# Performance work log

Hardware: AMD Instinct MI355X
Metric: run time of the kernel (lower is better)

## Reference

```python
import jax, jax.numpy as jnp
import numpy as np

B, S, D, F, E, SH, K = 2, 2048, 2048, 1024, 16, 2, 2


def setup_inputs() -> dict:
    key = jax.random.key(0)
    ks = jax.random.split(key, 8)
    std = 0.02
    mk = lambda k, sh: (jax.random.normal(k, sh, jnp.float32) * std)
    return {
        "x": jax.random.normal(ks[0], (B, S, D), jnp.float32),
        "wa": mk(ks[1], (D, E)),                      # router, no bias
        "rg": mk(ks[2], (E, D, F)), "rgb": jnp.zeros((E, F), jnp.float32),
        "rw1": mk(ks[3], (E, D, F)), "rb1": jnp.zeros((E, F), jnp.float32),
        "rw2": mk(ks[4], (E, F, D)), "rb2": jnp.zeros((E, D), jnp.float32),
        "sg": mk(ks[5], (SH, D, F)), "sgb": jnp.zeros((SH, F), jnp.float32),
        "sw1": mk(ks[6], (SH, D, F)), "sb1": jnp.zeros((SH, F), jnp.float32),
        "sw2": mk(ks[7], (SH, F, D)), "sb2": jnp.zeros((SH, D), jnp.float32),
    }


def _experts_all(x, g, gb, w1, b1, w2, b2):
    """Run every expert in the stack on every token.
    x: [b,s,d]; g,w1: [e,d,f]; w2: [e,f,d] -> out [b,s,e,d].
    Expert: w2( gelu(gated(x)) * w1(x) ). torch GELU default = exact erf.
    """
    y = jax.nn.gelu(jnp.einsum('bsd,edf->bsef', x, g) + gb, approximate=False)
    y = y * (jnp.einsum('bsd,edf->bsef', x, w1) + b1)
    return jnp.einsum('bsef,efd->bsed', y, w2) + b2


def reference(x, wa, rg, rgb, rw1, rb1, rw2, rb2, sg, sgb, sw1, sb1, sw2, sb2):
    # sigmoid affinity router + top-k, renormalized over the k selected
    aff = jax.nn.sigmoid(jnp.einsum('bsd,de->bse', x, wa))
    topk_p, topk_i = jax.lax.top_k(aff, K)                   # [b,s,k]
    topk_p = topk_p / jnp.sum(topk_p, axis=-1, keepdims=True)
    # dense combine weights [b,s,E]; zero for unselected experts, so the
    # masked-scatter of the original is reproduced exactly by a weighted sum
    combine = jnp.sum(jax.nn.one_hot(topk_i, E, dtype=x.dtype) * topk_p[..., None], axis=2)
    routed = jnp.einsum('bsed,bse->bsd',
                        _experts_all(x, rg, rgb, rw1, rb1, rw2, rb2), combine)
    shared = jnp.sum(_experts_all(x, sg, sgb, sw1, sb1, sw2, sb2), axis=2)
    return x + shared + routed
```

## Files before the change

### kernel.cpp

```cpp
#include <hip/hip_runtime.h>
#include <hip/hip_bf16.h>
#include <math.h>

typedef __bf16 bf16;
typedef bf16  bf16x8 __attribute__((ext_vector_type(8)));
typedef bf16  bf16x4 __attribute__((ext_vector_type(4)));
typedef float f32x4  __attribute__((ext_vector_type(4)));

#define TOKENS 4096
#define DM 2048
#define FF 1024
#define NE 16
#define SH_BASE 12288
#define BK 64

#define WS_CNT    0
#define WS_POS    64
#define WS_BASE   128
#define WS_TOPKW  256
#define WS_TOPKI  33024
#define WS_TSLOT  65792
#define WS_LIST   98560
#define WS_XB     180480
#define WS_H      16957696
#define WS_Y      58900736
#define WS_B1R    142786816
#define WS_B1S    277004544
#define WS_W2TR   293781760
#define WS_W2TS   360890624

__device__ __forceinline__ bf16 f2bf(float f) {
  unsigned u = __builtin_bit_cast(unsigned, f);
  u += 0x7fffu + ((u >> 16) & 1u);
  unsigned short h = (unsigned short)(u >> 16);
  return __builtin_bit_cast(bf16, h);
}

typedef const __attribute__((address_space(1))) void* gas_t;
typedef __attribute__((address_space(3))) void* las_t;
__device__ __forceinline__ void load_lds16(const bf16* g, bf16* l) {
  __builtin_amdgcn_global_load_lds((gas_t)g, (las_t)l, 16, 0, 0);
}

__global__ void transpose_cvt_all_kernel(const float* __restrict__ rw2, const float* __restrict__ sw2,
                                         bf16* __restrict__ W2TR, bf16* __restrict__ W2TS) {
  __shared__ float tile[64][65];
  const int z = blockIdx.z;
  const float* src_base;
  bf16* dst_base;
  if (z < NE) { src_base = rw2 + (size_t)z * FF * DM; dst_base = W2TR + (size_t)z * DM * FF; }
  else { const int s = z - NE; src_base = sw2 + (size_t)s * FF * DM; dst_base = W2TS + (size_t)s * DM * FF; }
  const int R = FF, C = DM;
  const int c0 = blockIdx.x * 64, r0 = blockIdx.y * 64;
  const int t = threadIdx.x;
  const int lr = t >> 2;
  const int lc = (t & 3) * 4;
  const float* src = src_base + (size_t)(r0 + lr) * C + c0;
#pragma unroll
  for (int j = 0; j < 4; j++) {
    const f32x4 v = *(const f32x4*)(src + lc + j * 16);
    tile[lr][lc + j * 16 + 0] = v[0];
    tile[lr][lc + j * 16 + 1] = v[1];
    tile[lr][lc + j * 16 + 2] = v[2];
    tile[lr][lc + j * 16 + 3] = v[3];
  }
  __syncthreads();
  const int co = t >> 4;
  const int ro = (t & 15) * 4;
#pragma unroll
  for (int j = 0; j < 4; j++) {
    const int c = co + j * 16;
    bf16x4 v;
    v[0] = f2bf(tile[ro + 0][c]);
    v[1] = f2bf(tile[ro + 1][c]);
    v[2] = f2bf(tile[ro + 2][c]);
    v[3] = f2bf(tile[ro + 3][c]);
    *(bf16x4*)(dst_base + (size_t)(c0 + c) * R + r0 + ro) = v;
  }
}

__global__ void transpose_cvt_fused_all_kernel(
    const float* __restrict__ rg, const float* __restrict__ rw1,
    const float* __restrict__ sg, const float* __restrict__ sw1,
    bf16* __restrict__ B1R, bf16* __restrict__ B1S) {
  __shared__ float tile[64][65];
  const int z = blockIdx.z;
  const int half = (z >= 18) ? 1 : 0;
  const int ze = z - 18 * half;
  const float* src_base;
  bf16* dst_base;
  if (ze < NE) {
    src_base = (half ? rw1 : rg) + (size_t)ze * DM * FF;
    dst_base = B1R + (size_t)ze * (2 * FF) * DM;
  } else {
    const int s = ze - NE;
    src_base = (half ? sw1 : sg) + (size_t)s * DM * FF;
    dst_base = B1S + (size_t)s * (2 * FF) * DM;
  }
  const int c0 = blockIdx.x * 64, r0 = blockIdx.y * 64;
  const int t = threadIdx.x;
  const int lr = t >> 2;
  const int lc = (t & 3) * 4;
  const float* src = src_base + (size_t)(r0 + lr) * FF + c0;
#pragma unroll
  for (int j = 0; j < 4; j++) {
    const f32x4 v = *(const f32x4*)(src + lc + j * 16);
    tile[lr][lc + j * 16 + 0] = v[0];
    tile[lr][lc + j * 16 + 1] = v[1];
    tile[lr][lc + j * 16 + 2] = v[2];
    tile[lr][lc + j * 16 + 3] = v[3];
  }
  __syncthreads();
  const int co = t >> 4;
  const int ro = (t & 15) * 4;
#pragma unroll
  for (int j = 0; j < 4; j++) {
    const int c = co + j * 16;
    const int f = c0 + c;
    const int fr = ((f >> 4) << 5) + half * 16 + (f & 15);
    bf16x4 v;
    v[0] = f2bf(tile[ro + 0][c]);
    v[1] = f2bf(tile[ro + 1][c]);
    v[2] = f2bf(tile[ro + 2][c]);
    v[3] = f2bf(tile[ro + 3][c]);
    *(bf16x4*)(dst_base + (size_t)fr * DM + r0 + ro) = v;
  }
}

#define RT_TOK 16
#define RT_DK  256
#define RT_PITCH (RT_DK + 4)

__global__ __launch_bounds__(256) void router_kernel(
    const float* __restrict__ x, const float* __restrict__ wa,
    float* __restrict__ topk_w, int* __restrict__ topk_i,
    int* __restrict__ cnt, bf16* __restrict__ xb) {
  __shared__ float xs[RT_TOK][RT_PITCH];
  __shared__ float was[NE][RT_PITCH];
  __shared__ float aff[RT_TOK][17];

  const int tid = threadIdx.x;
  const int t = tid >> 4;
  const int e = tid & 15;
  const int t0 = blockIdx.x * RT_TOK;

  f32x4 acc4 = {0.f, 0.f, 0.f, 0.f};

  for (int d0 = 0; d0 < DM; d0 += RT_DK) {
    __syncthreads();
    {
      const int r = tid >> 4;
      const int c4 = (tid & 15) * 4;
      const float* src = x + (size_t)(t0 + r) * DM + d0;
      bf16* dstx = xb + (size_t)(t0 + r) * DM + d0;
#pragma unroll
      for (int j = 0; j < 4; j++) {
        const f32x4 v = *(const f32x4*)(src + c4 + j * 64);
        *(f32x4*)(&xs[r][c4 + j * 64]) = v;
        bf16x4 o;
        o[0] = f2bf(v[0]); o[1] = f2bf(v[1]); o[2] = f2bf(v[2]); o[3] = f2bf(v[3]);
        *(bf16x4*)(dstx + c4 + j * 64) = o;
      }
    }
    {
      const int e2 = tid & 15;
      const int dd = (tid >> 4) * 16;
#pragma unroll
      for (int j = 0; j < 16; j++)
        was[e2][dd + j] = wa[(size_t)(d0 + dd + j) * NE + e2];
    }
    __syncthreads();
#pragma unroll 16
    for (int d = 0; d < RT_DK; d += 4) {
      const f32x4 xv = *(const f32x4*)(&xs[t][d]);
      const f32x4 wv = *(const f32x4*)(&was[e][d]);
      acc4 += xv * wv;
    }
  }

  const float a = acc4[0] + acc4[1] + acc4[2] + acc4[3];
  aff[t][e] = 1.f / (1.f + expf(-a));
  __syncthreads();

  if (e == 0) {
    float b0 = -1e30f, b1 = -1e30f; int i0 = 0, i1 = 0;
    for (int i = 0; i < NE; i++) {
      const float v = aff[t][i];
      if (v > b0) { b1 = b0; i1 = i0; b0 = v; i0 = i; }
      else if (v > b1) { b1 = v; i1 = i; }
    }
    const int tok = t0 + t;
    const float inv = 1.f / (b0 + b1);
    topk_w[tok * 2] = b0 * inv;  topk_w[tok * 2 + 1] = b1 * inv;
    topk_i[tok * 2] = i0;        topk_i[tok * 2 + 1] = i1;
    atomicAdd(&cnt[i0], 1);      atomicAdd(&cnt[i1], 1);
  }
}

__global__ void prefix_kernel(const int* __restrict__ cnt, int* __restrict__ base) {
  if (threadIdx.x == 0) {
    int acc = 0;
    for (int e = 0; e < NE; e++) { base[e] = acc; acc += (cnt[e] + 127) & ~127; }
    base[NE] = SH_BASE;
    base[NE + 1] = SH_BASE + TOKENS;
  }
}

__global__ void build_lists_kernel(const int* __restrict__ topk_i, const int* __restrict__ base,
                                   int* __restrict__ pos, int* __restrict__ list,
                                   int* __restrict__ token_slot) {
  const int t = blockIdx.x * 256 + threadIdx.x;
  if (t >= TOKENS) return;
#pragma unroll
  for (int k = 0; k < 2; k++) {
    const int e = topk_i[t * 2 + k];
    const int p = atomicAdd(&pos[e], 1);
    const int slot = base[e] + p;
    list[slot] = t;
    token_slot[t * 2 + k] = slot;
  }
  list[SH_BASE + t] = t;
  list[SH_BASE + TOKENS + t] = t;
}

#define GEMM_GRID_MAX 2304

__device__ __forceinline__ bool map_tile(int flat, const int* __restrict__ cnt,
                                         int& e, int& my, int& nx) {
  int o = 0;
  for (int ee = 0; ee < NE + 2; ++ee) {
    const int ce = (ee < NE) ? cnt[ee] : TOKENS;
    const int me = (ce + 127) >> 7;
    const int Te = me << 4;
    if (flat < o + Te) {
      const int l = flat - o;
      const int s = (l & 7) * (me << 1) + (l >> 3);
      nx = s / me;
      my = s - nx * me;
      e = ee;
      return true;
    }
    o += Te;
  }
  return false;
}

__global__ __launch_bounds__(256, 2) void gemm1_kernel(
    const bf16* __restrict__ xb, const int* __restrict__ list,
    const int* __restrict__ base, const int* __restrict__ cnt,
    const bf16* __restrict__ B1R, const bf16* __restrict__ B1S,
    const float* __restrict__ rgb, const float* __restrict__ rb1,
    const float* __restrict__ sgb, const float* __restrict__ sb1,
    bf16* __restrict__ H) {
  int e, bmy, bnx;
  if (!map_tile(blockIdx.x, cnt, e, bmy, bnx)) return;
  const int ce = (e < NE) ? cnt[e] : TOKENS;
  const int m0 = bmy * 128;
  const int n0 = bnx * 128;
  const int bse = base[e];

  const bf16* B1; const float *gb, *ub;
  if (e < NE) { B1 = B1R + (size_t)e * (2 * FF) * DM; gb = rgb + e * FF; ub = rb1 + e * FF; }
  else { const int s = e - NE; B1 = B1S + (size_t)s * (2 * FF) * DM; gb = sgb + s * FF; ub = sb1 + s * FF; }

  __shared__ bf16 As[2][128 * BK];
  __shared__ bf16 Bs[2][128 * BK];

  const int tid = threadIdx.x, lane = tid & 63, wid = tid >> 6;
  const int lrow = lane >> 3;
  const int laneK = (((lane & 7) ^ lrow) << 3);
  const int q0 = wid << 5;

  const bf16* aP[4];
#pragma unroll
  for (int i = 0; i < 4; i++) {
    int rA = m0 + q0 + (i << 3) + lrow;
    if (rA >= ce) rA = ce - 1;
    aP[i] = xb + (size_t)list[bse + rA] * DM + laneK;
  }
  const bf16* bP = B1 + (size_t)(n0 + q0 + lrow) * DM + laneK;

  const int wm = (wid & 1) * 64, wn = (wid >> 1) * 64;
  const int m16 = lane & 15, quad = lane >> 4, xor7 = m16 & 7;

  f32x4 acc[4][4] = {};

#pragma unroll
  for (int i = 0; i < 4; i++) {
    load_lds16(aP[i], &As[0][(q0 + (i << 3)) * BK + (lane << 3)]);
    load_lds16(bP + (size_t)(i * 8) * DM, &Bs[0][(q0 + (i << 3)) * BK + (lane << 3)]);
  }

  int cur = 0;
  for (int k0 = 0; k0 < DM; k0 += BK) {
    __syncthreads();
    if (k0 + BK < DM) {
      const int nxt = cur ^ 1;
      const int kn = k0 + BK;
#pragma unroll
      for (int i = 0; i < 4; i++) {
        load_lds16(aP[i] + kn, &As[nxt][(q0 + (i << 3)) * BK + (lane << 3)]);
        load_lds16(bP + (size_t)(i * 8) * DM + kn, &Bs[nxt][(q0 + (i << 3)) * BK + (lane << 3)]);
      }
    }
#pragma unroll
    for (int kk = 0; kk < 2; kk++) {
      const int slot = (((kk << 2) + quad) ^ xor7) << 3;
      bf16x8 af[4], bfr[4];
#pragma unroll
      for (int i = 0; i < 4; i++) {
        af[i]  = *(const bf16x8*)(&As[cur][(wm + m16 + 16 * i) * BK + slot]);
        bfr[i] = *(const bf16x8*)(&Bs[cur][(wn + m16 + 16 * i) * BK + slot]);
      }
#pragma unroll
      for (int mi = 0; mi < 4; mi++)
#pragma unroll
        for (int ni = 0; ni < 4; ni++)
          acc[mi][ni] = __builtin_amdgcn_mfma_f32_16x16x32_bf16(af[mi], bfr[ni], acc[mi][ni], 0, 0, 0);
    }
    cur ^= 1;
  }

  const int q4 = quad * 4;
  const int fbase = ((n0 + wn) >> 1) + m16;
#pragma unroll
  for (int mi = 0; mi < 4; mi++) {
#pragma unroll
    for (int nj = 0; nj < 2; nj++) {
      const int f = fbase + nj * 16;
      const float gbv = gb[f], ubv = ub[f];
#pragma unroll
      for (int r = 0; r < 4; r++) {
        const int row = m0 + wm + mi * 16 + q4 + r;
        const float g = acc[mi][2 * nj][r] + gbv;
        const float u = acc[mi][2 * nj + 1][r] + ubv;
        const float h = 0.5f * g * (1.f + erff(g * 0.70710678118f)) * u;
        H[(size_t)(bse + row) * FF + f] = f2bf(h);
      }
    }
  }
}

__global__ __launch_bounds__(256, 2) void gemm2_kernel(
    const bf16* __restrict__ Hb, const int* __restrict__ base, const int* __restrict__ cnt,
    const bf16* __restrict__ rw2T, const bf16* __restrict__ sw2T,
    const float* __restrict__ rb2, const float* __restrict__ sb2,
    bf16* __restrict__ Y) {
  int e, bmy, bnx;
  if (!map_tile(blockIdx.x, cnt, e, bmy, bnx)) return;
  const int m0 = bmy * 128;
  const int n0 = bnx * 128;
  const int bse = base[e];

  const bf16* B; const float* bb;
  if (e < NE) { B = rw2T + (size_t)e * DM * FF; bb = rb2 + e * DM; }
  else { const int s = e - NE; B = sw2T + (size_t)s * DM * FF; bb = sb2 + s * DM; }

  __shared__ bf16 As[2][128 * BK];
  __shared__ bf16 Bs[2][128 * BK];

  const int tid = threadIdx.x, lane = tid & 63, wid = tid >> 6;
  const int lrow = lane >> 3;
  const int laneK = (((lane & 7) ^ lrow) << 3);
  const int q0 = wid << 5;

  const bf16* aP = Hb + (size_t)(bse + m0 + q0 + lrow) * FF + laneK;
  const bf16* bP = B  + (size_t)(n0 + q0 + lrow) * FF + laneK;

  const int wm = (wid & 1) * 64, wn = (wid >> 1) * 64;
  const int m16 = lane & 15, quad = lane >> 4, xor7 = m16 & 7;

  f32x4 acc[4][4] = {};

#pragma unroll
  for (int i = 0; i < 4; i++) {
    load_lds16(aP + (size_t)(i * 8) * FF, &As[0][(q0 + (i << 3)) * BK + (lane << 3)]);
    load_lds16(bP + (size_t)(i * 8) * FF, &Bs[0][(q0 + (i << 3)) * BK + (lane << 3)]);
  }

  int cur = 0;
  for (int k0 = 0; k0 < FF; k0 += BK) {
    __syncthreads();
    if (k0 + BK < FF) {
      const int nxt = cur ^ 1;
      const int kn = k0 + BK;
#pragma unroll
      for (int i = 0; i < 4; i++) {
        load_lds16(aP + (size_t)(i * 8) * FF + kn, &As[nxt][(q0 + (i << 3)) * BK + (lane << 3)]);
        load_lds16(bP + (size_t)(i * 8) * FF + kn, &Bs[nxt][(q0 + (i << 3)) * BK + (lane << 3)]);
      }
    }
#pragma unroll
    for (int kk = 0; kk < 2; kk++) {
      const int slot = (((kk << 2) + quad) ^ xor7) << 3;
      bf16x8 af[4], bfr[4];
#pragma unroll
      for (int i = 0; i < 4; i++) {
        af[i]  = *(const bf16x8*)(&As[cur][(wm + m16 + 16 * i) * BK + slot]);
        bfr[i] = *(const bf16x8*)(&Bs[cur][(wn + m16 + 16 * i) * BK + slot]);
      }
#pragma unroll
      for (int mi = 0; mi < 4; mi++)
#pragma unroll
        for (int ni = 0; ni < 4; ni++)
          acc[mi][ni] = __builtin_amdgcn_mfma_f32_16x16x32_bf16(af[mi], bfr[ni], acc[mi][ni], 0, 0, 0);
    }
    cur ^= 1;
  }

  const int q4 = quad * 4;
#pragma unroll
  for (int mi = 0; mi < 4; mi++) {
#pragma unroll
    for (int ni = 0; ni < 4; ni++) {
      const int n = n0 + wn + ni * 16 + m16;
      const float bv = bb[n];
#pragma unroll
      for (int r = 0; r < 4; r++) {
        const int row = m0 + wm + mi * 16 + q4 + r;
        Y[(size_t)(bse + row) * DM + n] = f2bf(acc[mi][ni][r] + bv);
      }
    }
  }
}

__global__ void combine_kernel(const float* __restrict__ x, const bf16* __restrict__ Y,
                               const int* __restrict__ token_slot, const float* __restrict__ topk_w,
                               float* __restrict__ out) {
  const int t = blockIdx.x;
  const int d = threadIdx.x * 8;
  const int s0 = token_slot[t * 2], s1 = token_slot[t * 2 + 1];
  const float w0 = topk_w[t * 2], w1 = topk_w[t * 2 + 1];
  const bf16x8 ya = *(const bf16x8*)(Y + (size_t)(SH_BASE + t) * DM + d);
  const bf16x8 yb = *(const bf16x8*)(Y + (size_t)(SH_BASE + TOKENS + t) * DM + d);
  const bf16x8 y0 = *(const bf16x8*)(Y + (size_t)s0 * DM + d);
  const bf16x8 y1 = *(const bf16x8*)(Y + (size_t)s1 * DM + d);
  const float* xp = x + (size_t)t * DM + d;
  float* op = out + (size_t)t * DM + d;
#pragma unroll
  for (int j = 0; j < 8; j++)
    op[j] = xp[j] + (float)ya[j] + (float)yb[j] + w0 * (float)y0[j] + w1 * (float)y1[j];
}

extern "C" void kernel_launch(void* const* d_in, const int* in_sizes, int n_in,
                              void* d_out, int out_size, void* d_ws, size_t ws_size,
                              hipStream_t stream) {
  (void)in_sizes; (void)n_in; (void)out_size; (void)ws_size;
  const float* x   = (const float*)d_in[0];
  const float* wa  = (const float*)d_in[1];
  const float* rg  = (const float*)d_in[2];
  const float* rgb = (const float*)d_in[3];
  const float* rw1 = (const float*)d_in[4];
  const float* rb1 = (const float*)d_in[5];
  const float* rw2 = (const float*)d_in[6];
  const float* rb2 = (const float*)d_in[7];
  const float* sg  = (const float*)d_in[8];
  const float* sgb = (const float*)d_in[9];
  const float* sw1 = (const float*)d_in[10];
  const float* sb1 = (const float*)d_in[11];
  const float* sw2 = (const float*)d_in[12];
  const float* sb2 = (const float*)d_in[13];
  float* out = (float*)d_out;

  char* ws = (char*)d_ws;
  int*   cnt        = (int*)(ws + WS_CNT);
  int*   pos        = (int*)(ws + WS_POS);
  int*   basep      = (int*)(ws + WS_BASE);
  float* topk_w     = (float*)(ws + WS_TOPKW);
  int*   topk_i     = (int*)(ws + WS_TOPKI);
  int*   token_slot = (int*)(ws + WS_TSLOT);
  int*   list       = (int*)(ws + WS_LIST);
  bf16*  xb         = (bf16*)(ws + WS_XB);
  bf16*  H          = (bf16*)(ws + WS_H);
  bf16*  Y          = (bf16*)(ws + WS_Y);
  bf16*  B1R        = (bf16*)(ws + WS_B1R);
  bf16*  B1S        = (bf16*)(ws + WS_B1S);
  bf16*  W2TR       = (bf16*)(ws + WS_W2TR);
  bf16*  W2TS       = (bf16*)(ws + WS_W2TS);

  hipMemsetAsync(ws, 0, 128, stream);

  router_kernel<<<TOKENS / RT_TOK, 256, 0, stream>>>(x, wa, topk_w, topk_i, cnt, xb);
  prefix_kernel<<<1, 64, 0, stream>>>(cnt, basep);
  build_lists_kernel<<<TOKENS / 256, 256, 0, stream>>>(topk_i, basep, pos, list, token_slot);

  transpose_cvt_fused_all_kernel<<<dim3(FF / 64, DM / 64, 36), 256, 0, stream>>>(
      rg, rw1, sg, sw1, B1R, B1S);
  transpose_cvt_all_kernel<<<dim3(DM / 64, FF / 64, 18), 256, 0, stream>>>(
      rw2, sw2, W2TR, W2TS);

  gemm1_kernel<<<GEMM_GRID_MAX, 256, 0, stream>>>(
      xb, list, basep, cnt, B1R, B1S, rgb, rb1, sgb, sb1, H);
  gemm2_kernel<<<GEMM_GRID_MAX, 256, 0, stream>>>(
      H, basep, cnt, W2TR, W2TS, rb2, sb2, Y);
  combine_kernel<<<TOKENS, 256, 0, stream>>>(x, Y, token_slot, topk_w, out);
}
```

Measured before the change: 906.4 us.

## Use 256x256 tiles with 8 waves and 4-stage pipelined loads in expert GEMMs

Both grouped GEMMs move from 128x128 tiles with 4 waves and a double-buffered BK=64 loop to 256x256 tiles with 8 waves, a BK=32 K-step and a 4-deep LDS ring buffer. Explicit vmcnt waits and raw barriers replace __syncthreads, and s_setprio wraps the MFMA block. Expert segments are padded to 256 rows so the tile mapping stays valid. The goal is more operand reuse per byte loaded and better hiding of global-load latency. The cost is more padding waste on small experts, fewer blocks (640 max) and higher register and LDS pressure, which may limit occupancy.

Result: slower. 962.2 us (+6.2%).

```diff
diff --git a/kernel.cpp b/kernel.cpp
--- a/kernel.cpp
+++ b/kernel.cpp
@@ -12,7 +12,6 @@
 #define FF 1024
 #define NE 16
 #define SH_BASE 12288
-#define BK 64
 
 #define WS_CNT    0
 #define WS_POS    64
@@ -200,7 +199,7 @@
 __global__ void prefix_kernel(const int* __restrict__ cnt, int* __restrict__ base) {
   if (threadIdx.x == 0) {
     int acc = 0;
-    for (int e = 0; e < NE; e++) { base[e] = acc; acc += (cnt[e] + 127) & ~127; }
+    for (int e = 0; e < NE; e++) { base[e] = acc; acc += (cnt[e] + 255) & ~255; }
     base[NE] = SH_BASE;
     base[NE + 1] = SH_BASE + TOKENS;
   }
@@ -223,20 +222,18 @@
   list[SH_BASE + TOKENS + t] = t;
 }
 
-#define GEMM_GRID_MAX 2304
-
-__device__ __forceinline__ bool map_tile(int flat, const int* __restrict__ cnt,
-                                         int& e, int& my, int& nx) {
+#define GEMM_GRID_MAX 640
+
+__device__ __forceinline__ bool map_tile256(int flat, const int* __restrict__ cnt,
+                                            int& e, int& my, int& nx) {
   int o = 0;
   for (int ee = 0; ee < NE + 2; ++ee) {
     const int ce = (ee < NE) ? cnt[ee] : TOKENS;
-    const int me = (ce + 127) >> 7;
-    const int Te = me << 4;
+    const int me = (ce + 255) >> 8;
+    const int Te = me << 3;
     if (flat < o + Te) {
-      const int l = flat - o;
-      const int s = (l & 7) * (me << 1) + (l >> 3);
-      nx = s / me;
-      my = s - nx * me;
+      my = (flat - o) >> 3;
+      nx = flat & 7;
       e = ee;
       return true;
     }
@@ -245,7 +242,8 @@
   return false;
 }
 
-__global__ __launch_bounds__(256, 2) void gemm1_kernel(
+
+__global__ __launch_bounds__(512, 2) void gemm1_kernel(
     const bf16* __restrict__ xb, const int* __restrict__ list,
     const int* __restrict__ base, const int* __restrict__ cnt,
     const bf16* __restrict__ B1R, const bf16* __restrict__ B1S,
@@ -253,85 +251,87 @@
     const float* __restrict__ sgb, const float* __restrict__ sb1,
     bf16* __restrict__ H) {
   int e, bmy, bnx;
-  if (!map_tile(blockIdx.x, cnt, e, bmy, bnx)) return;
+  if (!map_tile256(blockIdx.x, cnt, e, bmy, bnx)) return;
   const int ce = (e < NE) ? cnt[e] : TOKENS;
-  const int m0 = bmy * 128;
-  const int n0 = bnx * 128;
+  const int m0 = bmy * 256;
+  const int n0 = bnx * 256;
   const int bse = base[e];
 
   const bf16* B1; const float *gb, *ub;
   if (e < NE) { B1 = B1R + (size_t)e * (2 * FF) * DM; gb = rgb + e * FF; ub = rb1 + e * FF; }
   else { const int s = e - NE; B1 = B1S + (size_t)s * (2 * FF) * DM; gb = sgb + s * FF; ub = sb1 + s * FF; }
 
-  __shared__ bf16 As[2][128 * BK];
-  __shared__ bf16 Bs[2][128 * BK];
+  __shared__ bf16 As[4][8192];
+  __shared__ bf16 Bs[4][8192];
 
   const int tid = threadIdx.x, lane = tid & 63, wid = tid >> 6;
-  const int lrow = lane >> 3;
-  const int laneK = (((lane & 7) ^ lrow) << 3);
-  const int q0 = wid << 5;
-
-  const bf16* aP[4];
-#pragma unroll
-  for (int i = 0; i < 4; i++) {
-    int rA = m0 + q0 + (i << 3) + lrow;
-    if (rA >= ce) rA = ce - 1;
-    aP[i] = xb + (size_t)list[bse + rA] * DM + laneK;
-  }
-  const bf16* bP = B1 + (size_t)(n0 + q0 + lrow) * DM + laneK;
-
-  const int wm = (wid & 1) * 64, wn = (wid >> 1) * 64;
-  const int m16 = lane & 15, quad = lane >> 4, xor7 = m16 & 7;
-
-  f32x4 acc[4][4] = {};
-
-#pragma unroll
-  for (int i = 0; i < 4; i++) {
-    load_lds16(aP[i], &As[0][(q0 + (i << 3)) * BK + (lane << 3)]);
-    load_lds16(bP + (size_t)(i * 8) * DM, &Bs[0][(q0 + (i << 3)) * BK + (lane << 3)]);
-  }
-
-  int cur = 0;
-  for (int k0 = 0; k0 < DM; k0 += BK) {
-    __syncthreads();
-    if (k0 + BK < DM) {
-      const int nxt = cur ^ 1;
-      const int kn = k0 + BK;
-#pragma unroll
-      for (int i = 0; i < 4; i++) {
-        load_lds16(aP[i] + kn, &As[nxt][(q0 + (i << 3)) * BK + (lane << 3)]);
-        load_lds16(bP + (size_t)(i * 8) * DM + kn, &Bs[nxt][(q0 + (i << 3)) * BK + (lane << 3)]);
-      }
-    }
-#pragma unroll
-    for (int kk = 0; kk < 2; kk++) {
-      const int slot = (((kk << 2) + quad) ^ xor7) << 3;
-      bf16x8 af[4], bfr[4];
-#pragma unroll
-      for (int i = 0; i < 4; i++) {
-        af[i]  = *(const bf16x8*)(&As[cur][(wm + m16 + 16 * i) * BK + slot]);
-        bfr[i] = *(const bf16x8*)(&Bs[cur][(wn + m16 + 16 * i) * BK + slot]);
-      }
-#pragma unroll
-      for (int mi = 0; mi < 4; mi++)
-#pragma unroll
-        for (int ni = 0; ni < 4; ni++)
-          acc[mi][ni] = __builtin_amdgcn_mfma_f32_16x16x32_bf16(af[mi], bfr[ni], acc[mi][ni], 0, 0, 0);
-    }
-    cur ^= 1;
-  }
+  const int m16 = lane & 15, quad = lane >> 4;
+  const int wml = (wid & 1) * 128, wnl = (wid >> 1) * 64;
+  const int rslot = ((quad ^ ((m16 >> 1) & 3)) << 3);
+
+  const int rl0 = wid * 32 + (lane >> 2);
+  const int rl1 = rl0 + 16;
+  const int gsw = (((lane & 3) ^ ((lane >> 3) & 3)) << 3);
+  int ra0 = m0 + rl0; if (ra0 >= ce) ra0 = ce - 1;
+  int ra1 = m0 + rl1; if (ra1 >= ce) ra1 = ce - 1;
+  const bf16* aS0 = xb + (size_t)list[bse + ra0] * DM + gsw;
+  const bf16* aS1 = xb + (size_t)list[bse + ra1] * DM + gsw;
+  const bf16* bS0 = B1 + (size_t)(n0 + rl0) * DM + gsw;
+  const bf16* bS1 = B1 + (size_t)(n0 + rl1) * DM + gsw;
+  const int awb = wid * 1024;
+
+  f32x4 acc[8][4] = {};
+
+#define G1_STAGE(b, kof)                          \
+  {                                               \
+    load_lds16(aS0 + (kof), &As[b][awb]);         \
+    load_lds16(aS1 + (kof), &As[b][awb + 512]);   \
+    load_lds16(bS0 + (kof), &Bs[b][awb]);         \
+    load_lds16(bS1 + (kof), &Bs[b][awb + 512]);   \
+  }
+
+  G1_STAGE(0, 0)
+  G1_STAGE(1, 32)
+  G1_STAGE(2, 64)
+  asm volatile("s_waitcnt vmcnt(8)" ::: "memory");
+  __builtin_amdgcn_s_barrier();
+
+  const int NT = DM / 32;
+  for (int t = 0; t < NT; ++t) {
+    const int cb = t & 3;
+    if (t + 3 < NT) { const int nb = (t + 3) & 3; G1_STAGE(nb, (t + 3) * 32) }
+    bf16x8 af[8], bv[4];
+#pragma unroll
+    for (int i = 0; i < 8; i++)
+      af[i] = *(const bf16x8*)(&As[cb][(wml + m16 + 16 * i) * 32 + rslot]);
+#pragma unroll
+    for (int j = 0; j < 4; j++)
+      bv[j] = *(const bf16x8*)(&Bs[cb][(wnl + m16 + 16 * j) * 32 + rslot]);
+    __builtin_amdgcn_s_setprio(1);
+#pragma unroll
+    for (int mi = 0; mi < 8; mi++)
+#pragma unroll
+      for (int ni = 0; ni < 4; ni++)
+        acc[mi][ni] = __builtin_amdgcn_mfma_f32_16x16x32_bf16(af[mi], bv[ni], acc[mi][ni], 0, 0, 0);
+    __builtin_amdgcn_s_setprio(0);
+    if (t < NT - 3)       asm volatile("s_waitcnt vmcnt(8)" ::: "memory");
+    else if (t == NT - 3) asm volatile("s_waitcnt vmcnt(4)" ::: "memory");
+    else if (t == NT - 2) asm volatile("s_waitcnt vmcnt(0)" ::: "memory");
+    if (t < NT - 1) __builtin_amdgcn_s_barrier();
+  }
+#undef G1_STAGE
 
   const int q4 = quad * 4;
-  const int fbase = ((n0 + wn) >> 1) + m16;
-#pragma unroll
-  for (int mi = 0; mi < 4; mi++) {
+  const int fbase = ((n0 + wnl) >> 1) + m16;
+#pragma unroll
+  for (int mi = 0; mi < 8; mi++) {
 #pragma unroll
     for (int nj = 0; nj < 2; nj++) {
       const int f = fbase + nj * 16;
       const float gbv = gb[f], ubv = ub[f];
 #pragma unroll
       for (int r = 0; r < 4; r++) {
-        const int row = m0 + wm + mi * 16 + q4 + r;
+        const int row = m0 + wml + mi * 16 + q4 + r;
         const float g = acc[mi][2 * nj][r] + gbv;
         const float u = acc[mi][2 * nj + 1][r] + ubv;
         const float h = 0.5f * g * (1.f + erff(g * 0.70710678118f)) * u;
@@ -341,84 +341,90 @@
   }
 }
 
-__global__ __launch_bounds__(256, 2) void gemm2_kernel(
+__global__ __launch_bounds__(512, 2) void gemm2_kernel(
     const bf16* __restrict__ Hb, const int* __restrict__ base, const int* __restrict__ cnt,
     const bf16* __restrict__ rw2T, const bf16* __restrict__ sw2T,
     const float* __restrict__ rb2, const float* __restrict__ sb2,
     bf16* __restrict__ Y) {
   int e, bmy, bnx;
-  if (!map_tile(blockIdx.x, cnt, e, bmy, bnx)) return;
-  const int m0 = bmy * 128;
-  const int n0 = bnx * 128;
+  if (!map_tile256(blockIdx.x, cnt, e, bmy, bnx)) return;
+  const int m0 = bmy * 256;
+  const int n0 = bnx * 256;
   const int bse = base[e];
 
   const bf16* B; const float* bb;
   if (e < NE) { B = rw2T + (size_t)e * DM * FF; bb = rb2 + e * DM; }
   else { const int s = e - NE; B = sw2T + (size_t)s * DM * FF; bb = sb2 + s * DM; }
 
-  __shared__ bf16 As[2][128 * BK];
-  __shared__ bf16 Bs[2][128 * BK];
+  __shared__ bf16 As[4][8192];
+  __shared__ bf16 Bs[4][8192];
 
   const int tid = threadIdx.x, lane = tid & 63, wid = tid >> 6;
-  const int lrow = lane >> 3;
-  const int laneK = (((lane & 7) ^ lrow) << 3);
-  const int q0 = wid << 5;
-
-  const bf16* aP = Hb + (size_t)(bse + m0 + q0 + lrow) * FF + laneK;
-  const bf16* bP = B  + (size_t)(n0 + q0 + lrow) * FF + laneK;
-
-  const int wm = (wid & 1) * 64, wn = (wid >> 1) * 64;
-  const int m16 = lane & 15, quad = lane >> 4, xor7 = m16 & 7;
-
-  f32x4 acc[4][4] = {};
-
-#pragma unroll
-  for (int i = 0; i < 4; i++) {
-    load_lds16(aP + (size_t)(i * 8) * FF, &As[0][(q0 + (i << 3)) * BK + (lane << 3)]);
-    load_lds16(bP + (size_t)(i * 8) * FF, &Bs[0][(q0 + (i << 3)) * BK + (lane << 3)]);
-  }
-
-  int cur = 0;
-  for (int k0 = 0; k0 < FF; k0 += BK) {
-    __syncthreads();
-    if (k0 + BK < FF) {
-      const int nxt = cur ^ 1;
-      const int kn = k0 + BK;
-#pragma unroll
-      for (int i = 0; i < 4; i++) {
-        load_lds16(aP + (size_t)(i * 8) * FF + kn, &As[nxt][(q0 + (i << 3)) * BK + (lane << 3)]);
-        load_lds16(bP + (size_t)(i * 8) * FF + kn, &Bs[nxt][(q0 + (i << 3)) * BK + (lane << 3)]);
-      }
-    }
-#pragma unroll
-    for (int kk = 0; kk < 2; kk++) {
-      const int slot = (((kk << 2) + quad) ^ xor7) << 3;
-      bf16x8 af[4], bfr[4];
-#pragma unroll
-      for (int i = 0; i < 4; i++) {
-        af[i]  = *(const bf16x8*)(&As[cur][(wm + m16 + 16 * i) * BK + slot]);
-        bfr[i] = *(const bf16x8*)(&Bs[cur][(wn + m16 + 16 * i) * BK + slot]);
-      }
-#pragma unroll
-      for (int mi = 0; mi < 4; mi++)
-#pragma unroll
-        for (int ni = 0; ni < 4; ni++)
-          acc[mi][ni] = __builtin_amdgcn_mfma_f32_16x16x32_bf16(af[mi], bfr[ni], acc[mi][ni], 0, 0, 0);
-    }
-    cur ^= 1;
-  }
+  const int m16 = lane & 15, quad = lane >> 4;
+  const int wml = (wid & 1) * 128, wnl = (wid >> 1) * 64;
+  const int rslot = ((quad ^ ((m16 >> 1) & 3)) << 3);
+
+  const int rl0 = wid * 32 + (lane >> 2);
+  const int rl1 = rl0 + 16;
+  const int gsw = (((lane & 3) ^ ((lane >> 3) & 3)) << 3);
+  const bf16* aS0 = Hb + (size_t)(bse + m0 + rl0) * FF + gsw;
+  const bf16* aS1 = Hb + (size_t)(bse + m0 + rl1) * FF + gsw;
+  const bf16* bS0 = B + (size_t)(n0 + rl0) * FF + gsw;
+  const bf16* bS1 = B + (size_t)(n0 + rl1) * FF + gsw;
+  const int awb = wid * 1024;
+
+  f32x4 acc[8][4] = {};
+
+#define G2_STAGE(b, kof)                          \
+  {                                               \
+    load_lds16(aS0 + (kof), &As[b][awb]);         \
+    load_lds16(aS1 + (kof), &As[b][awb + 512]);   \
+    load_lds16(bS0 + (kof), &Bs[b][awb]);         \
+    load_lds16(bS1 + (kof), &Bs[b][awb + 512]);   \
+  }
+
+  G2_STAGE(0, 0)
+  G2_STAGE(1, 32)
+  G2_STAGE(2, 64)
+  asm volatile("s_waitcnt vmcnt(8)" ::: "memory");
+  __builtin_amdgcn_s_barrier();
+
+  const int NT = FF / 32;
+  for (int t = 0; t < NT; ++t) {
+    const int cb = t & 3;
+    if (t + 3 < NT) { const int nb = (t + 3) & 3; G2_STAGE(nb, (t + 3) * 32) }
+    bf16x8 af[8], bv[4];
+#pragma unroll
+    for (int i = 0; i < 8; i++)
+      af[i] = *(const bf16x8*)(&As[cb][(wml + m16 + 16 * i) * 32 + rslot]);
+#pragma unroll
+    for (int j = 0; j < 4; j++)
+      bv[j] = *(const bf16x8*)(&Bs[cb][(wnl + m16 + 16 * j) * 32 + rslot]);
+    __builtin_amdgcn_s_setprio(1);
+#pragma unroll
+    for (int mi = 0; mi < 8; mi++)
+#pragma unroll
+      for (int ni = 0; ni < 4; ni++)
+        acc[mi][ni] = __builtin_amdgcn_mfma_f32_16x16x32_bf16(af[mi], bv[ni], acc[mi][ni], 0, 0, 0);
+    __builtin_amdgcn_s_setprio(0);
+    if (t < NT - 3)       asm volatile("s_waitcnt vmcnt(8)" ::: "memory");
+    else if (t == NT - 3) asm volatile("s_waitcnt vmcnt(4)" ::: "memory");
+    else if (t == NT - 2) asm volatile("s_waitcnt vmcnt(0)" ::: "memory");
+    if (t < NT - 1) __builtin_amdgcn_s_barrier();
+  }
+#undef G2_STAGE
 
   const int q4 = quad * 4;
 #pragma unroll
-  for (int mi = 0; mi < 4; mi++) {
+  for (int mi = 0; mi < 8; mi++) {
 #pragma unroll
     for (int ni = 0; ni < 4; ni++) {
-      const int n = n0 + wn + ni * 16 + m16;
-      const float bv = bb[n];
+      const int n = n0 + wnl + ni * 16 + m16;
+      const float bv2 = bb[n];
 #pragma unroll
       for (int r = 0; r < 4; r++) {
-        const int row = m0 + wm + mi * 16 + q4 + r;
-        Y[(size_t)(bse + row) * DM + n] = f2bf(acc[mi][ni][r] + bv);
+        const int row = m0 + wml + mi * 16 + q4 + r;
+        Y[(size_t)(bse + row) * DM + n] = f2bf(acc[mi][ni][r] + bv2);
       }
     }
   }
@@ -489,9 +495,9 @@
   transpose_cvt_all_kernel<<<dim3(DM / 64, FF / 64, 18), 256, 0, stream>>>(
       rw2, sw2, W2TR, W2TS);
 
-  gemm1_kernel<<<GEMM_GRID_MAX, 256, 0, stream>>>(
+  gemm1_kernel<<<GEMM_GRID_MAX, 512, 0, stream>>>(
       xb, list, basep, cnt, B1R, B1S, rgb, rb1, sgb, sb1, H);
-  gemm2_kernel<<<GEMM_GRID_MAX, 256, 0, stream>>>(
+  gemm2_kernel<<<GEMM_GRID_MAX, 512, 0, stream>>>(
       H, basep, cnt, W2TR, W2TS, rb2, sb2, Y);
   combine_kernel<<<TOKENS, 256, 0, stream>>>(x, Y, token_slot, topk_w, out);
 }
```
